# Optimization experiments

Measured on AMD Instinct MI355X. Metric: run time of the kernel, lower is better.

The kernel has to match this reference:

```python
import jax, jax.numpy as jnp
import numpy as np

EMBED_DIM = 2048
NUM_HEADS = 16
HEAD_DIM = EMBED_DIM // NUM_HEADS
BATCH = 4
SEQ = 1024
ROPE_BASE = 10000.0


def _rotate_half(x):
    x1, x2 = jnp.split(x, 2, axis=-1)
    return jnp.concatenate([-x2, x1], axis=-1)


def setup_inputs() -> dict:
    key = jax.random.key(0)
    ks = jax.random.split(key, 8)
    query = jax.random.normal(ks[0], (BATCH, SEQ, EMBED_DIM), dtype=jnp.float32)
    kkey = jax.random.normal(ks[1], (BATCH, SEQ, EMBED_DIM), dtype=jnp.float32)
    value = jax.random.normal(ks[2], (BATCH, SEQ, EMBED_DIM), dtype=jnp.float32)
    # causal mask: scores.masked_fill(mask == 0, -inf)
    mask = jnp.tril(jnp.ones((SEQ, SEQ), dtype=jnp.int32))[None, None]
    # RoPE tables [S, head_dim]
    inv_freq = 1.0 / (ROPE_BASE ** (np.arange(0, HEAD_DIM, 2, dtype=np.float32) / HEAD_DIM))
    pos = np.arange(SEQ, dtype=np.float32)
    freqs = np.outer(pos, inv_freq)                      # [S, D/2]
    emb = np.concatenate([freqs, freqs], axis=-1)        # [S, D]
    rope_cos = jnp.asarray(np.cos(emb), dtype=jnp.float32)
    rope_sin = jnp.asarray(np.sin(emb), dtype=jnp.float32)
    s = 1.0 / np.sqrt(EMBED_DIM)
    Wq = jax.random.normal(ks[3], (EMBED_DIM, EMBED_DIM), dtype=jnp.float32) * s
    Wk = jax.random.normal(ks[4], (EMBED_DIM, EMBED_DIM), dtype=jnp.float32) * s
    Wv = jax.random.normal(ks[5], (EMBED_DIM, EMBED_DIM), dtype=jnp.float32) * s
    Wo = jax.random.normal(ks[6], (EMBED_DIM, EMBED_DIM), dtype=jnp.float32) * s
    return {"query": query, "key": kkey, "value": value, "mask": mask,
            "rope_cos": rope_cos, "rope_sin": rope_sin,
            "Wq": Wq, "Wk": Wk, "Wv": Wv, "Wo": Wo}


def reference(query, key, value, mask, rope_cos, rope_sin, Wq, Wk, Wv, Wo):
    B, S, E = query.shape
    # projections (nn.Linear: x @ W.T)
    def proj(x, W):
        y = x @ W.T
        return y.reshape(B, -1, NUM_HEADS, HEAD_DIM).transpose(0, 2, 1, 3)  # [B,H,S,D]
    Q = proj(query, Wq)
    K = proj(key, Wk)
    V = proj(value, Wv)
    # RoPE (rotate-half form), cos/sin broadcast over batch and heads
    cos = rope_cos[None, None]  # [1,1,S,D]
    sin = rope_sin[None, None]
    Q = Q * cos + _rotate_half(Q) * sin
    K = K * cos + _rotate_half(K) * sin
    scale = jnp.asarray(np.sqrt(HEAD_DIM), dtype=Q.dtype)
    scores = jnp.einsum('bhqd,bhkd->bhqk', Q, K) / scale
    scores = jnp.where(mask == 0, jnp.asarray(-jnp.inf, scores.dtype), scores)
    attn = jax.nn.softmax(scores, axis=-1)
    context = jnp.einsum('bhqk,bhkd->bhqd', attn, V)
    context = context.transpose(0, 2, 1, 3).reshape(B, S, E)
    out = context @ Wo.T
    return out
```

## Files before the change

kernel.cpp:

```cpp
#include <hip/hip_runtime.h>
#include <stdint.h>

#define E_DIM 2048
#define N_HEADS 16
#define H_DIM 128
#define BATCH 4
#define SEQL 1024
#define M_ROWS 4096

typedef __attribute__((ext_vector_type(8))) short bf16x8;
typedef __attribute__((ext_vector_type(4))) float f32x4;

#define AS1 __attribute__((address_space(1)))
#define AS3 __attribute__((address_space(3)))

__device__ __forceinline__ void gload16(const void* g, void* l) {
  __builtin_amdgcn_global_load_lds((const AS1 uint32_t*)g, (AS3 uint32_t*)l, 16, 0, 0);
}

__device__ __forceinline__ unsigned short f2bf(float f) {
  union { float f; uint32_t u; } v; v.f = f;
  return (unsigned short)((v.u + 0x7FFFu + ((v.u >> 16) & 1u)) >> 16);
}

__global__ __launch_bounds__(256) void k_cvt(
    const float* __restrict__ q, const float* __restrict__ k, const float* __restrict__ v,
    const float* __restrict__ wq, const float* __restrict__ wk,
    const float* __restrict__ wv, const float* __restrict__ wo,
    ushort* __restrict__ oq, ushort* __restrict__ ok, ushort* __restrict__ ov,
    ushort* __restrict__ owq, ushort* __restrict__ owk,
    ushort* __restrict__ owv, ushort* __restrict__ owo) {
  int y = blockIdx.y;
  const float* in;
  ushort* out;
  if (y < 3) {
    in = (y == 0) ? q : (y == 1) ? k : v;
    out = (y == 0) ? oq : (y == 1) ? ok : ov;
  } else {
    if (blockIdx.x >= 4096) return;
    in = (y == 3) ? wq : (y == 4) ? wk : (y == 5) ? wv : wo;
    out = (y == 3) ? owq : (y == 4) ? owk : (y == 5) ? owv : owo;
  }
  int i = (blockIdx.x * 256 + threadIdx.x) * 4;
  float4 vv = *reinterpret_cast<const float4*>(in + i);
  *reinterpret_cast<ushort4*>(out + i) =
      make_ushort4(f2bf(vv.x), f2bf(vv.y), f2bf(vv.z), f2bf(vv.w));
}

template <int NREP>
__device__ __forceinline__ void gemm256_mainloop(const ushort* __restrict__ A,
                                                 const ushort* __restrict__ W,
                                                 ushort* lds, int m0, int n0,
                                                 const int browRows[NREP],
                                                 f32x4 (&acc)[8][NREP]) {
  const int tid = threadIdx.x;
  const int w = tid >> 6, lane = tid & 63, quad = lane >> 4, lid = lane & 15;
  constexpr int BELE = NREP * 4096;
  ushort* bufA[2] = {lds, lds + 16384};
  ushort* bufB[2] = {lds + 32768, lds + 32768 + BELE};

  const int p0 = tid, p1i = tid + 512;
  const int r0 = p0 >> 3, c0 = (p0 & 7) ^ (r0 & 7);
  const int r1 = p1i >> 3, c1 = (p1i & 7) ^ (r1 & 7);
  const int ld0 = (w * 64) * 8;
  const int ld1 = (512 + w * 64) * 8;

  const ushort* gA = A + (size_t)m0 * E_DIM;
  const ushort* gB = W + (size_t)n0 * E_DIM;

  auto stage = [&](const ushort* g, ushort* buf, int kt, int half) {
    const ushort* s0p = g + (size_t)(half * 128 + r0) * E_DIM + kt * 64 + c0 * 8;
    const ushort* s1p = g + (size_t)(half * 128 + r1) * E_DIM + kt * 64 + c1 * 8;
    ushort* l = buf + half * 8192;
    gload16(s0p, l + ld0);
    gload16(s1p, l + ld1);
  };

  int ofsA[2], ofsB[NREP][2];
  {
    const int rowA = (w >> 2) * 128 + lid;
#pragma unroll
    for (int ks = 0; ks < 2; ++ks)
      ofsA[ks] = rowA * 64 + (((ks * 4 + quad) ^ (lid & 7)) * 8);
#pragma unroll
    for (int ni = 0; ni < NREP; ++ni)
#pragma unroll
      for (int ks = 0; ks < 2; ++ks)
        ofsB[ni][ks] = browRows[ni] * 64 + (((ks * 4 + quad) ^ (lid & 7)) * 8);
  }

  bf16x8 bfr[NREP][2];

#define VMW_N                                                                  \
  do {                                                                         \
    if constexpr (NREP == 4)                                                   \
      asm volatile("s_waitcnt vmcnt(4)" ::: "memory");                         \
    else                                                                       \
      asm volatile("s_waitcnt vmcnt(2)" ::: "memory");                         \
  } while (0)

#define PH(b, q, STGS, VMW)                                                    \
  do {                                                                         \
    bf16x8 af[2][2];                                                           \
    if ((q) == 0) {                                                            \
      _Pragma("unroll") for (int ni = 0; ni < NREP; ++ni)                      \
          _Pragma("unroll") for (int ks = 0; ks < 2; ++ks)                     \
              bfr[ni][ks] =                                                    \
                  *reinterpret_cast<const bf16x8*>(bufB[b] + ofsB[ni][ks]);    \
    }                                                                          \
    _Pragma("unroll") for (int d = 0; d < 2; ++d)                              \
        _Pragma("unroll") for (int ks = 0; ks < 2; ++ks)                       \
            af[d][ks] = *reinterpret_cast<const bf16x8*>(                      \
                bufA[b] + ofsA[ks] + ((q) * 2 + d) * 1024);                    \
    STGS;                                                                      \
    VMW;                                                                       \
    __builtin_amdgcn_s_barrier();                                              \
    asm volatile("s_waitcnt lgkmcnt(0)" ::: "memory");                         \
    __builtin_amdgcn_s_setprio(1);                                             \
    _Pragma("unroll") for (int ks = 0; ks < 2; ++ks)                           \
        _Pragma("unroll") for (int d = 0; d < 2; ++d)                          \
            _Pragma("unroll") for (int ni = 0; ni < NREP; ++ni)                \
                acc[(q) * 2 + d][ni] = __builtin_amdgcn_mfma_f32_16x16x32_bf16(\
                    af[d][ks], bfr[ni][ks], acc[(q) * 2 + d][ni], 0, 0, 0);    \
    __builtin_amdgcn_s_setprio(0);                                             \
    __builtin_amdgcn_s_barrier();                                              \
  } while (0)

  stage(gB, bufB[0], 0, 0); if (NREP == 4) stage(gB, bufB[0], 0, 1);
  stage(gA, bufA[0], 0, 0); stage(gA, bufA[0], 0, 1);
  stage(gB, bufB[1], 1, 0); if (NREP == 4) stage(gB, bufB[1], 1, 1);
  VMW_N;
  __builtin_amdgcn_s_barrier();

  for (int i = 0; i < 16; ++i) {
    const bool lastI = (i == 15);
    const int tn = 2 * i;
    PH(0, 0, stage(gA, bufA[1], tn + 1, 0), );
    PH(0, 1, stage(gA, bufA[1], tn + 1, 1), );
    PH(0, 2, if (!lastI) stage(gB, bufB[0], tn + 2, 0), );
    PH(0, 3, if (!lastI && NREP == 4) stage(gB, bufB[0], tn + 2, 1),
       if (lastI) asm volatile("s_waitcnt vmcnt(0)" ::: "memory");
       else VMW_N);
    PH(1, 0, if (!lastI) stage(gA, bufA[0], tn + 2, 0), );
    PH(1, 1, if (!lastI) stage(gA, bufA[0], tn + 2, 1), );
    PH(1, 2, if (!lastI) stage(gB, bufB[1], tn + 3, 0), );
    PH(1, 3, if (!lastI && NREP == 4) stage(gB, bufB[1], tn + 3, 1),
       if (!lastI) VMW_N);
  }
#undef PH
#undef VMW_N
}

__global__ __launch_bounds__(512, 2) void k_gemm_qkv(
    const ushort* __restrict__ xq, const ushort* __restrict__ xk, const ushort* __restrict__ xv,
    const ushort* __restrict__ wq, const ushort* __restrict__ wk, const ushort* __restrict__ wv,
    ushort* __restrict__ Qr, ushort* __restrict__ Kr, ushort* __restrict__ Vt,
    const float* __restrict__ cosT, const float* __restrict__ sinT) {
  extern __shared__ ushort lds[];
  const int z = blockIdx.z;
  const ushort* A = (z == 0) ? xq : (z == 1) ? xk : xv;
  const ushort* W = (z == 0) ? wq : (z == 1) ? wk : wv;
  const int tid = threadIdx.x;
  const int w = tid >> 6, lane = tid & 63, quad = lane >> 4, lid = lane & 15;
  const int wn = w & 3;
  const int n0 = blockIdx.x * 256;
  const int m0 = blockIdx.y * 256;

  int browRows[4];
#pragma unroll
  for (int ni = 0; ni < 4; ++ni)
    browRows[ni] = (wn >> 1) * 128 + (wn & 1) * 32 + (ni & 1) * 16 + (ni >> 1) * 64 + lid;

  f32x4 acc[8][4];
  const f32x4 z4 = {0.f, 0.f, 0.f, 0.f};
#pragma unroll
  for (int i = 0; i < 8; ++i)
#pragma unroll
    for (int j = 0; j < 4; ++j) acc[i][j] = z4;

  gemm256_mainloop<4>(A, W, lds, m0, n0, browRows, acc);

  const int b = m0 >> 10;
  if (z < 2) {
    ushort* Out = (z == 0) ? Qr : Kr;
    const int h = blockIdx.x * 2 + (wn >> 1);
    ushort* Og = Out + (size_t)(b * N_HEADS + h) * SEQL * H_DIM;
#pragma unroll
    for (int mi = 0; mi < 8; ++mi)
#pragma unroll
      for (int r = 0; r < 4; ++r) {
        int s = (m0 & (SEQL - 1)) + (w >> 2) * 128 + mi * 16 + quad * 4 + r;
        size_t row = (size_t)s * H_DIM;
#pragma unroll
        for (int ni = 0; ni < 2; ++ni) {
          int d0 = (wn & 1) * 32 + ni * 16 + lid;
          float c = cosT[s * H_DIM + d0];
          float sn = sinT[s * H_DIM + d0];
          float x0 = acc[mi][ni][r], x1 = acc[mi][ni + 2][r];
          Og[row + d0]      = f2bf(x0 * c - x1 * sn);
          Og[row + d0 + 64] = f2bf(x1 * c + x0 * sn);
        }
      }
  } else {
    __syncthreads();
    ushort* T = lds;
    const int sl0 = (w >> 2) * 128 + quad * 4;
#pragma unroll
    for (int mi = 0; mi < 8; ++mi)
#pragma unroll
      for (int ni = 0; ni < 4; ++ni) {
        ushort4 pk;
        pk.x = f2bf(acc[mi][ni][0]);
        pk.y = f2bf(acc[mi][ni][1]);
        pk.z = f2bf(acc[mi][ni][2]);
        pk.w = f2bf(acc[mi][ni][3]);
        *reinterpret_cast<ushort4*>(T + browRows[ni] * 264 + sl0 + mi * 16) = pk;
      }
    __syncthreads();
    const int sg = (m0 & (SEQL - 1));
#pragma unroll
    for (int r32 = 0; r32 < 32; ++r32) {
      int c = w * 32 + r32;
      int d = c & 127;
      int h = blockIdx.x * 2 + (c >> 7);
      ushort4 v4 = *reinterpret_cast<const ushort4*>(T + c * 264 + lane * 4);
      *reinterpret_cast<ushort4*>(
          Vt + ((size_t)((b * N_HEADS + h) * H_DIM + d)) * SEQL + sg + lane * 4) = v4;
    }
  }
}

__global__ __launch_bounds__(512, 2) void k_gemm_o(const ushort* __restrict__ A,
                                                   const ushort* __restrict__ W,
                                                   float* __restrict__ Out) {
  extern __shared__ ushort lds[];
  const int tid = threadIdx.x;
  const int w = tid >> 6, lane = tid & 63, quad = lane >> 4, lid = lane & 15;
  const int wn = w & 3;
  const int n0 = blockIdx.x * 128;
  const int m0 = blockIdx.y * 256;

  int browRows[2];
#pragma unroll
  for (int ni = 0; ni < 2; ++ni) browRows[ni] = wn * 32 + ni * 16 + lid;

  f32x4 acc[8][2];
  const f32x4 z4 = {0.f, 0.f, 0.f, 0.f};
#pragma unroll
  for (int i = 0; i < 8; ++i)
#pragma unroll
    for (int j = 0; j < 2; ++j) acc[i][j] = z4;

  gemm256_mainloop<2>(A, W, lds, m0, n0, browRows, acc);

#pragma unroll
  for (int mi = 0; mi < 8; ++mi)
#pragma unroll
    for (int r = 0; r < 4; ++r) {
      size_t row = (size_t)(m0 + (w >> 2) * 128 + mi * 16 + quad * 4 + r) * E_DIM + n0;
#pragma unroll
      for (int ni = 0; ni < 2; ++ni) Out[row + browRows[ni]] = acc[mi][ni][r];
    }
}

__global__ __launch_bounds__(256, 2) void k_attn(const ushort* __restrict__ Q,
                                                 const ushort* __restrict__ K,
                                                 const ushort* __restrict__ Vt,
                                                 ushort* __restrict__ Ctx) {
  extern __shared__ ushort lds[];
  const int tid = threadIdx.x;
  const int w = tid >> 6, lane = tid & 63, quad = lane >> 4, lid = lane & 15;
  ushort* Pw = lds + 32768 + w * 1280;

  const int l = blockIdx.y * 8 + blockIdx.x;
  const int g = (l & 1) ^ ((l >> 8) & 1);
  const int base = (l >> 1) & 7;
  const int qt = g ? 7 - base : base;
  const int bh = ((l >> 4) & 31) | (g << 5);
  const int q0 = qt * 128;
  const size_t bse = (size_t)bh * SEQL * H_DIM;
  const ushort* Qg = Q + bse;
  const ushort* Kg = K + bse;
  const ushort* Vg = Vt + bse;

  auto stageK = [&](ushort* dst, int j0) {
#pragma unroll
    for (int i = 0; i < 4; ++i) {
      int g2 = i * 256 + tid;
      int kk = g2 >> 4;
      int c = (g2 & 15) ^ (kk & 15);
      gload16(Kg + (size_t)(j0 + kk) * H_DIM + c * 8, dst + (i * 256 + w * 64) * 8);
    }
  };
  auto stageV = [&](ushort* dst, int j0) {
#pragma unroll
    for (int i = 0; i < 4; ++i) {
      int g2 = i * 256 + tid;
      int d = g2 >> 3;
      int c = (g2 & 7) ^ (d & 7);
      gload16(Vg + (size_t)d * SEQL + j0 + c * 8, dst + (i * 256 + w * 64) * 8);
    }
  };

  bf16x8 qf[2][4];
  for (int mt = 0; mt < 2; ++mt) {
    int row = q0 + w * 32 + mt * 16 + lid;
    for (int kc = 0; kc < 4; ++kc)
      qf[mt][kc] = *reinterpret_cast<const bf16x8*>(Qg + (size_t)row * H_DIM + kc * 32 + quad * 8);
  }

  f32x4 oacc[2][8];
  f32x4 lacc[2];
  const f32x4 z4 = {0.f, 0.f, 0.f, 0.f};
  for (int mt = 0; mt < 2; ++mt) {
    lacc[mt] = z4;
    for (int dt = 0; dt < 8; ++dt) oacc[mt][dt] = z4;
  }

  bf16x8 ones;
  for (int i = 0; i < 8; ++i) ones[i] = (short)0x3F80;

  const float SC2 = 0.08838834764831845f * 1.4426950408889634f;
  const float M2 = 12.0f * 1.4426950408889634f;

  ushort *Kc = lds, *Kn = lds + 8192;
  ushort *Vc = lds + 16384, *Vn = lds + 24576;

  const int NT = (q0 >> 6) + 2;
  stageK(Kc, 0);
  stageV(Vc, 0);
  __syncthreads();

  for (int t = 0; t < NT; ++t) {
    const int j0 = t << 6;
    if (t + 1 < NT) { stageK(Kn, j0 + 64); stageV(Vn, j0 + 64); }

    f32x4 sacc[2][4];
    for (int mt = 0; mt < 2; ++mt)
      for (int nt = 0; nt < 4; ++nt) sacc[mt][nt] = z4;
    __builtin_amdgcn_s_setprio(1);
    for (int kc = 0; kc < 4; ++kc)
      for (int nt = 0; nt < 4; ++nt) {
        int kk = nt * 16 + lid;
        bf16x8 kf = *reinterpret_cast<const bf16x8*>(
            Kc + kk * H_DIM + (((kc * 4 + quad) ^ lid) * 8));
        sacc[0][nt] = __builtin_amdgcn_mfma_f32_16x16x32_bf16(qf[0][kc], kf, sacc[0][nt], 0, 0, 0);
        sacc[1][nt] = __builtin_amdgcn_mfma_f32_16x16x32_bf16(qf[1][kc], kf, sacc[1][nt], 0, 0, 0);
      }
    __builtin_amdgcn_s_setprio(0);

    if (j0 + 64 > q0) {
      for (int mt = 0; mt < 2; ++mt)
        for (int nt = 0; nt < 4; ++nt)
          for (int r = 0; r < 4; ++r) {
            int key = j0 + nt * 16 + lid;
            int row = q0 + w * 32 + mt * 16 + quad * 4 + r;
            if (key > row) sacc[mt][nt][r] = -3.0e38f;
          }
    }

    for (int h4 = 0; h4 < 2; ++h4) {
      for (int mt = 0; mt < 2; ++mt)
        for (int half = 0; half < 2; ++half) {
          int nt = h4 * 2 + half;
          for (int r = 0; r < 4; ++r) {
            float p = exp2f(fmaf(sacc[mt][nt][r], SC2, -M2));
            Pw[(mt * 16 + quad * 4 + r) * 40 + half * 16 + lid] = f2bf(p);
          }
        }
      bf16x8 pf0 = *reinterpret_cast<const bf16x8*>(Pw + lid * 40 + quad * 8);
      bf16x8 pf1 = *reinterpret_cast<const bf16x8*>(Pw + (16 + lid) * 40 + quad * 8);
      lacc[0] = __builtin_amdgcn_mfma_f32_16x16x32_bf16(pf0, ones, lacc[0], 0, 0, 0);
      lacc[1] = __builtin_amdgcn_mfma_f32_16x16x32_bf16(pf1, ones, lacc[1], 0, 0, 0);
      __builtin_amdgcn_s_setprio(1);
      for (int dt = 0; dt < 8; ++dt) {
        int d = dt * 16 + lid;
        bf16x8 vf = *reinterpret_cast<const bf16x8*>(
            Vc + d * 64 + (((h4 * 4 + quad) ^ (d & 7)) * 8));
        oacc[0][dt] = __builtin_amdgcn_mfma_f32_16x16x32_bf16(pf0, vf, oacc[0][dt], 0, 0, 0);
        oacc[1][dt] = __builtin_amdgcn_mfma_f32_16x16x32_bf16(pf1, vf, oacc[1][dt], 0, 0, 0);
      }
      __builtin_amdgcn_s_setprio(0);
    }

    __syncthreads();
    ushort* t0 = Kc; Kc = Kn; Kn = t0;
    ushort* t1 = Vc; Vc = Vn; Vn = t1;
  }

  const int b = bh >> 4, h = bh & 15;
  for (int mt = 0; mt < 2; ++mt)
    for (int r = 0; r < 4; ++r) {
      int s = q0 + w * 32 + mt * 16 + quad * 4 + r;
      float inv = 1.0f / lacc[mt][r];
      for (int dt = 0; dt < 8; ++dt)
        Ctx[(size_t)(b * SEQL + s) * E_DIM + h * H_DIM + dt * 16 + lid] =
            f2bf(oacc[mt][dt][r] * inv);
    }
}

extern "C" void kernel_launch(void* const* d_in, const int* in_sizes, int n_in,
                              void* d_out, int out_size, void* d_ws, size_t ws_size,
                              hipStream_t stream) {
  const float* q_in = (const float*)d_in[0];
  const float* k_in = (const float*)d_in[1];
  const float* v_in = (const float*)d_in[2];
  const float* rc = (const float*)d_in[4];
  const float* rs = (const float*)d_in[5];
  const float* Wq = (const float*)d_in[6];
  const float* Wk = (const float*)d_in[7];
  const float* Wv = (const float*)d_in[8];
  const float* Wo = (const float*)d_in[9];
  float* out = (float*)d_out;

  ushort* p = (ushort*)d_ws;
  const size_t WSZ = (size_t)E_DIM * E_DIM;
  const size_t XSZ = (size_t)M_ROWS * E_DIM;
  ushort* wq_b = p; p += WSZ;
  ushort* wk_b = p; p += WSZ;
  ushort* wv_b = p; p += WSZ;
  ushort* wo_b = p; p += WSZ;
  ushort* xq_b = p; p += XSZ;
  ushort* xk_b = p; p += XSZ;
  ushort* xv_b = p; p += XSZ;
  ushort* Qr = p;   p += XSZ;
  ushort* Kr = p;   p += XSZ;
  ushort* Vt = p;   p += XSZ;
  ushort* ctx = xq_b;

  (void)hipFuncSetAttribute(reinterpret_cast<const void*>(k_gemm_qkv),
                            hipFuncAttributeMaxDynamicSharedMemorySize, 135168);
  (void)hipFuncSetAttribute(reinterpret_cast<const void*>(k_gemm_o),
                            hipFuncAttributeMaxDynamicSharedMemorySize, 98304);
  (void)hipFuncSetAttribute(reinterpret_cast<const void*>(k_attn),
                            hipFuncAttributeMaxDynamicSharedMemorySize, 75776);

  dim3 blk(256);
  k_cvt<<<dim3(8192, 7), blk, 0, stream>>>(q_in, k_in, v_in, Wq, Wk, Wv, Wo,
                                           xq_b, xk_b, xv_b, wq_b, wk_b, wv_b, wo_b);

  k_gemm_qkv<<<dim3(E_DIM / 256, M_ROWS / 256, 3), dim3(512), 135168, stream>>>(
      xq_b, xk_b, xv_b, wq_b, wk_b, wv_b, Qr, Kr, Vt, rc, rs);

  k_attn<<<dim3(8, BATCH * N_HEADS), blk, 75776, stream>>>(Qr, Kr, Vt, ctx);

  k_gemm_o<<<dim3(E_DIM / 128, M_ROWS / 256), dim3(512), 98304, stream>>>(ctx, wo_b, out);
}
```

Baseline: 385.3 us.

## Halve attention KV tile to 32 keys and swizzle V-transpose LDS staging

The attention kernel now processes 32 keys per iteration instead of 64. This shrinks the LDS double-buffers and dynamic shared memory so three blocks can reside per CU (launch bounds raised to 3), with the V tile swizzle adjusted to the narrower layout. Separately, the QKV GEMM's V-transpose epilogue uses an XOR-swizzled, unpadded 256-wide LDS layout with 16-byte reads and stores instead of padded 8-byte accesses, which lowers its LDS requirement. The trade-off is twice as many loop iterations and barriers in attention, each with less MFMA work to hide the global-load latency.

```diff
diff --git a/kernel.cpp b/kernel.cpp
--- a/kernel.cpp
+++ b/kernel.cpp
@@ -204,28 +204,32 @@
   } else {
     __syncthreads();
     ushort* T = lds;
-    const int sl0 = (w >> 2) * 128 + quad * 4;
-#pragma unroll
-    for (int mi = 0; mi < 8; ++mi)
+    const int hof = (quad & 1) * 4;
+    const int chb = (w >> 2) * 16 + (quad >> 1);
+#pragma unroll
+    for (int mi = 0; mi < 8; ++mi) {
+      const int ch = chb + mi * 2;
 #pragma unroll
       for (int ni = 0; ni < 4; ++ni) {
-        ushort4 pk;
-        pk.x = f2bf(acc[mi][ni][0]);
-        pk.y = f2bf(acc[mi][ni][1]);
-        pk.z = f2bf(acc[mi][ni][2]);
-        pk.w = f2bf(acc[mi][ni][3]);
-        *reinterpret_cast<ushort4*>(T + browRows[ni] * 264 + sl0 + mi * 16) = pk;
+        int row = browRows[ni];
+        ushort* dst = T + row * 256 + ((ch ^ (row & 7)) * 8) + hof;
+        uint lo = (uint)f2bf(acc[mi][ni][0]) | ((uint)f2bf(acc[mi][ni][1]) << 16);
+        uint hi = (uint)f2bf(acc[mi][ni][2]) | ((uint)f2bf(acc[mi][ni][3]) << 16);
+        *reinterpret_cast<uint*>(dst) = lo;
+        *reinterpret_cast<uint*>(dst + 2) = hi;
       }
+    }
     __syncthreads();
     const int sg = (m0 & (SEQL - 1));
-#pragma unroll
-    for (int r32 = 0; r32 < 32; ++r32) {
-      int c = w * 32 + r32;
+    const int ch = lane & 31;
+#pragma unroll
+    for (int it = 0; it < 16; ++it) {
+      int c = w * 32 + it * 2 + (lane >> 5);
       int d = c & 127;
       int h = blockIdx.x * 2 + (c >> 7);
-      ushort4 v4 = *reinterpret_cast<const ushort4*>(T + c * 264 + lane * 4);
-      *reinterpret_cast<ushort4*>(
-          Vt + ((size_t)((b * N_HEADS + h) * H_DIM + d)) * SEQL + sg + lane * 4) = v4;
+      bf16x8 v8 = *reinterpret_cast<const bf16x8*>(T + c * 256 + ((ch ^ (c & 7)) * 8));
+      *reinterpret_cast<bf16x8*>(
+          Vt + ((size_t)((b * N_HEADS + h) * H_DIM + d)) * SEQL + sg + ch * 8) = v8;
     }
   }
 }
@@ -263,14 +267,14 @@
     }
 }
 
-__global__ __launch_bounds__(256, 2) void k_attn(const ushort* __restrict__ Q,
+__global__ __launch_bounds__(256, 3) void k_attn(const ushort* __restrict__ Q,
                                                  const ushort* __restrict__ K,
                                                  const ushort* __restrict__ Vt,
                                                  ushort* __restrict__ Ctx) {
   extern __shared__ ushort lds[];
   const int tid = threadIdx.x;
   const int w = tid >> 6, lane = tid & 63, quad = lane >> 4, lid = lane & 15;
-  ushort* Pw = lds + 32768 + w * 1280;
+  ushort* Pw = lds + 16384 + w * 1280;
 
   const int l = blockIdx.y * 8 + blockIdx.x;
   const int g = (l & 1) ^ ((l >> 8) & 1);
@@ -285,7 +289,7 @@
 
   auto stageK = [&](ushort* dst, int j0) {
 #pragma unroll
-    for (int i = 0; i < 4; ++i) {
+    for (int i = 0; i < 2; ++i) {
       int g2 = i * 256 + tid;
       int kk = g2 >> 4;
       int c = (g2 & 15) ^ (kk & 15);
@@ -294,10 +298,10 @@
   };
   auto stageV = [&](ushort* dst, int j0) {
 #pragma unroll
-    for (int i = 0; i < 4; ++i) {
+    for (int i = 0; i < 2; ++i) {
       int g2 = i * 256 + tid;
-      int d = g2 >> 3;
-      int c = (g2 & 7) ^ (d & 7);
+      int d = g2 >> 2;
+      int c = (g2 & 3) ^ ((d ^ (d >> 2)) & 3);
       gload16(Vg + (size_t)d * SEQL + j0 + c * 8, dst + (i * 256 + w * 64) * 8);
     }
   };
@@ -323,24 +327,24 @@
   const float SC2 = 0.08838834764831845f * 1.4426950408889634f;
   const float M2 = 12.0f * 1.4426950408889634f;
 
-  ushort *Kc = lds, *Kn = lds + 8192;
-  ushort *Vc = lds + 16384, *Vn = lds + 24576;
-
-  const int NT = (q0 >> 6) + 2;
+  ushort *Kc = lds, *Kn = lds + 4096;
+  ushort *Vc = lds + 8192, *Vn = lds + 12288;
+
+  const int NT = (q0 >> 5) + 4;
   stageK(Kc, 0);
   stageV(Vc, 0);
   __syncthreads();
 
   for (int t = 0; t < NT; ++t) {
-    const int j0 = t << 6;
-    if (t + 1 < NT) { stageK(Kn, j0 + 64); stageV(Vn, j0 + 64); }
-
-    f32x4 sacc[2][4];
+    const int j0 = t << 5;
+    if (t + 1 < NT) { stageK(Kn, j0 + 32); stageV(Vn, j0 + 32); }
+
+    f32x4 sacc[2][2];
     for (int mt = 0; mt < 2; ++mt)
-      for (int nt = 0; nt < 4; ++nt) sacc[mt][nt] = z4;
+      for (int nt = 0; nt < 2; ++nt) sacc[mt][nt] = z4;
     __builtin_amdgcn_s_setprio(1);
     for (int kc = 0; kc < 4; ++kc)
-      for (int nt = 0; nt < 4; ++nt) {
+      for (int nt = 0; nt < 2; ++nt) {
         int kk = nt * 16 + lid;
         bf16x8 kf = *reinterpret_cast<const bf16x8*>(
             Kc + kk * H_DIM + (((kc * 4 + quad) ^ lid) * 8));
@@ -349,9 +353,9 @@
       }
     __builtin_amdgcn_s_setprio(0);
 
-    if (j0 + 64 > q0) {
+    if (j0 + 32 > q0) {
       for (int mt = 0; mt < 2; ++mt)
-        for (int nt = 0; nt < 4; ++nt)
+        for (int nt = 0; nt < 2; ++nt)
           for (int r = 0; r < 4; ++r) {
             int key = j0 + nt * 16 + lid;
             int row = q0 + w * 32 + mt * 16 + quad * 4 + r;
@@ -359,29 +363,25 @@
           }
     }
 
-    for (int h4 = 0; h4 < 2; ++h4) {
-      for (int mt = 0; mt < 2; ++mt)
-        for (int half = 0; half < 2; ++half) {
-          int nt = h4 * 2 + half;
-          for (int r = 0; r < 4; ++r) {
-            float p = exp2f(fmaf(sacc[mt][nt][r], SC2, -M2));
-            Pw[(mt * 16 + quad * 4 + r) * 40 + half * 16 + lid] = f2bf(p);
-          }
+    for (int mt = 0; mt < 2; ++mt)
+      for (int half = 0; half < 2; ++half)
+        for (int r = 0; r < 4; ++r) {
+          float p = exp2f(fmaf(sacc[mt][half][r], SC2, -M2));
+          Pw[(mt * 16 + quad * 4 + r) * 40 + half * 16 + lid] = f2bf(p);
         }
-      bf16x8 pf0 = *reinterpret_cast<const bf16x8*>(Pw + lid * 40 + quad * 8);
-      bf16x8 pf1 = *reinterpret_cast<const bf16x8*>(Pw + (16 + lid) * 40 + quad * 8);
-      lacc[0] = __builtin_amdgcn_mfma_f32_16x16x32_bf16(pf0, ones, lacc[0], 0, 0, 0);
-      lacc[1] = __builtin_amdgcn_mfma_f32_16x16x32_bf16(pf1, ones, lacc[1], 0, 0, 0);
-      __builtin_amdgcn_s_setprio(1);
-      for (int dt = 0; dt < 8; ++dt) {
-        int d = dt * 16 + lid;
-        bf16x8 vf = *reinterpret_cast<const bf16x8*>(
-            Vc + d * 64 + (((h4 * 4 + quad) ^ (d & 7)) * 8));
-        oacc[0][dt] = __builtin_amdgcn_mfma_f32_16x16x32_bf16(pf0, vf, oacc[0][dt], 0, 0, 0);
-        oacc[1][dt] = __builtin_amdgcn_mfma_f32_16x16x32_bf16(pf1, vf, oacc[1][dt], 0, 0, 0);
-      }
-      __builtin_amdgcn_s_setprio(0);
-    }
+    bf16x8 pf0 = *reinterpret_cast<const bf16x8*>(Pw + lid * 40 + quad * 8);
+    bf16x8 pf1 = *reinterpret_cast<const bf16x8*>(Pw + (16 + lid) * 40 + quad * 8);
+    lacc[0] = __builtin_amdgcn_mfma_f32_16x16x32_bf16(pf0, ones, lacc[0], 0, 0, 0);
+    lacc[1] = __builtin_amdgcn_mfma_f32_16x16x32_bf16(pf1, ones, lacc[1], 0, 0, 0);
+    __builtin_amdgcn_s_setprio(1);
+    for (int dt = 0; dt < 8; ++dt) {
+      int d = dt * 16 + lid;
+      bf16x8 vf = *reinterpret_cast<const bf16x8*>(
+          Vc + d * 32 + ((quad ^ ((d ^ (d >> 2)) & 3)) * 8));
+      oacc[0][dt] = __builtin_amdgcn_mfma_f32_16x16x32_bf16(pf0, vf, oacc[0][dt], 0, 0, 0);
+      oacc[1][dt] = __builtin_amdgcn_mfma_f32_16x16x32_bf16(pf1, vf, oacc[1][dt], 0, 0, 0);
+    }
+    __builtin_amdgcn_s_setprio(0);
 
     __syncthreads();
     ushort* t0 = Kc; Kc = Kn; Kn = t0;
@@ -429,20 +429,20 @@
   ushort* ctx = xq_b;
 
   (void)hipFuncSetAttribute(reinterpret_cast<const void*>(k_gemm_qkv),
-                            hipFuncAttributeMaxDynamicSharedMemorySize, 135168);
+                            hipFuncAttributeMaxDynamicSharedMemorySize, 131072);
   (void)hipFuncSetAttribute(reinterpret_cast<const void*>(k_gemm_o),
                             hipFuncAttributeMaxDynamicSharedMemorySize, 98304);
   (void)hipFuncSetAttribute(reinterpret_cast<const void*>(k_attn),
-                            hipFuncAttributeMaxDynamicSharedMemorySize, 75776);
+                            hipFuncAttributeMaxDynamicSharedMemorySize, 43008);
 
   dim3 blk(256);
   k_cvt<<<dim3(8192, 7), blk, 0, stream>>>(q_in, k_in, v_in, Wq, Wk, Wv, Wo,
                                            xq_b, xk_b, xv_b, wq_b, wk_b, wv_b, wo_b);
 
-  k_gemm_qkv<<<dim3(E_DIM / 256, M_ROWS / 256, 3), dim3(512), 135168, stream>>>(
+  k_gemm_qkv<<<dim3(E_DIM / 256, M_ROWS / 256, 3), dim3(512), 131072, stream>>>(
       xq_b, xk_b, xv_b, wq_b, wk_b, wv_b, Qr, Kr, Vt, rc, rs);
 
-  k_attn<<<dim3(8, BATCH * N_HEADS), blk, 75776, stream>>>(Qr, Kr, Vt, ctx);
+  k_attn<<<dim3(8, BATCH * N_HEADS), blk, 43008, stream>>>(Qr, Kr, Vt, ctx);
 
   k_gemm_o<<<dim3(E_DIM / 128, M_ROWS / 256), dim3(512), 98304, stream>>>(ctx, wo_b, out);
 }
```

After: 384.6 us. Within noise of the previous version (-0.2%).
